# Kernel tuning notes

Hardware: AMD Instinct MI355X
Metric: run time of the kernel (lower is better)

## Reference

```python
import jax, jax.numpy as jnp
import numpy as np

ROI_SIZE = 14  # hard-coded in the torch module


def _bilinear(feature, x, y):
    """feature: [B,C,H,W]; x, y: arbitrary (matching) shape S of sample coords.
    Returns [B, C, *S]. Matches torch code: corner indices are clamped BEFORE
    the interpolation weights are computed from them."""
    H, W = feature.shape[-2:]
    y1 = jnp.clip(jnp.floor(y).astype(jnp.int32), 0, H - 1)
    y2 = jnp.clip(jnp.floor(y).astype(jnp.int32) + 1, 0, H - 1)
    x1 = jnp.clip(jnp.floor(x).astype(jnp.int32), 0, W - 1)
    x2 = jnp.clip(jnp.floor(x).astype(jnp.int32) + 1, 0, W - 1)
    wx_lo = x - x1  # weight toward x2 column
    wx_hi = x2 - x  # weight toward x1 column
    wy_lo = y - y1
    wy_hi = y2 - y
    p = feature[:, :, y1, x1] * wx_hi + feature[:, :, y1, x2] * wx_lo
    q = feature[:, :, y2, x1] * wx_hi + feature[:, :, y2, x2] * wx_lo
    return p * wy_hi + q * wy_lo


def setup_inputs() -> dict:
    key = jax.random.key(0)
    kf, k1, k2, k3, k4 = jax.random.split(key, 5)
    B, C, H, W, R = 1, 256, 200, 320, 128
    feature = jax.random.normal(kf, (B, C, H, W), dtype=jnp.float32)
    y1 = jax.random.uniform(k1, (R,), minval=0.0, maxval=H * 0.5)
    x1 = jax.random.uniform(k2, (R,), minval=0.0, maxval=W * 0.5)
    hh = jax.random.uniform(k3, (R,), minval=8.0, maxval=H * 0.45)
    ww = jax.random.uniform(k4, (R,), minval=8.0, maxval=W * 0.45)
    rois = jnp.stack([y1, x1, y1 + hh, x1 + ww], axis=-1).astype(jnp.float32)
    return {"feature": feature, "rois": rois}


def reference(feature, rois):
    R = rois.shape[0]
    B, C, H, W = feature.shape
    sh = (rois[:, 2] - rois[:, 0]) / ROI_SIZE  # [R] bin height stride
    sw = (rois[:, 3] - rois[:, 1]) / ROI_SIZE  # [R] bin width stride
    m = jnp.arange(ROI_SIZE, dtype=rois.dtype)
    y_base = rois[:, 0:1] + sh[:, None] * m  # [R, M]
    x_base = rois[:, 1:2] + sw[:, None] * m  # [R, N]
    frac = jnp.array([1.0 / 3.0, 2.0 / 3.0], dtype=rois.dtype)
    ys = y_base[:, :, None] + sh[:, None, None] * frac  # [R, M, 2]
    xs = x_base[:, :, None] + sw[:, None, None] * frac  # [R, N, 2]
    # all 4 (y, x) sample-point combos per bin -> [R, M, N, 2, 2]
    yy = jnp.broadcast_to(ys[:, :, None, :, None], (R, ROI_SIZE, ROI_SIZE, 2, 2))
    xx = jnp.broadcast_to(xs[:, None, :, None, :], (R, ROI_SIZE, ROI_SIZE, 2, 2))
    samples = _bilinear(feature, xx, yy)  # [B, C, R, M, N, 2, 2]
    # Faithful to torch.max(tensor) with NO dim: global max over B, C, R and
    # the 4 sample points, giving one scalar per bin (m, n).
    bin_max = jnp.max(samples, axis=(0, 1, 2, 5, 6))  # [M, N]
    return jnp.broadcast_to(bin_max, (R, C, ROI_SIZE, ROI_SIZE))
```

## Files before the change

kernel.cpp:

```cpp
#include <hip/hip_runtime.h>
#include <float.h>
#include <stdint.h>

#define CC 256
#define HH 200
#define WW 320
#define HW (HH * WW)
#define MM 14
#define NCH 8
#define CG 4
#define CPB (CC / CG)
#define SP4 38
#define SPF (SP4 * 4)

__global__ void roi_init(float* __restrict__ binmax) {
    int t = blockIdx.x * blockDim.x + threadIdx.x;
    if (t < MM * MM) binmax[t] = -FLT_MAX;
}

__device__ inline void atomicMaxF(float* addr, float val) {
    if (val >= 0.0f) {
        atomicMax((int*)addr, __float_as_int(val));
    } else {
        atomicMin((unsigned int*)addr, __float_as_uint(val));
    }
}

__device__ __forceinline__ void gload_lds16(const float* g, float* l) {
    __builtin_amdgcn_global_load_lds(
        (const __attribute__((address_space(1))) unsigned int*)g,
        (__attribute__((address_space(3))) unsigned int*)l,
        16, 0, 0);
}

__global__ __launch_bounds__(256, 8) void roi_reduce(
    const float* __restrict__ feature,
    const float* __restrict__ rois,
    float* __restrict__ binmax)
{
    const int bid = blockIdx.x;
    const int cg  = bid & (CG - 1);
    const int rm  = bid >> 2;
    const int m   = rm % MM;
    const int r   = rm / MM;
    const int tid = threadIdx.x;
    const int cbase = cg * CPB;

    const float ry1 = rois[r * 4 + 0];
    const float rx1 = rois[r * 4 + 1];
    const float ry2 = rois[r * 4 + 2];
    const float rx2 = rois[r * 4 + 3];
    const float sh = (ry2 - ry1) * (1.0f / 14.0f);
    const float sw = (rx2 - rx1) * (1.0f / 14.0f);
    const float f13 = 1.0f / 3.0f, f23 = 2.0f / 3.0f;

    const float yA = ry1 + sh * (float)m + sh * f13;
    const float yB = ry1 + sh * (float)m + sh * f23;
    const int y1A = min(max((int)floorf(yA), 0), HH - 1);
    const int y2A = min(max((int)floorf(yA) + 1, 0), HH - 1);
    const int y1B = min(max((int)floorf(yB), 0), HH - 1);
    const int y2B = min(max((int)floorf(yB) + 1, 0), HH - 1);
    const float wyloA = yA - (float)y1A, wyhiA = (float)y2A - yA;
    const float wyloB = yB - (float)y1B, wyhiB = (float)y2B - yB;

    const float xmin = rx1 + sw * f13;
    const float xmax = rx1 + sw * 13.0f + sw * f23;
    int xlo = min(max((int)floorf(xmin), 0), WW - 1);
    int xhi = min(max((int)floorf(xmax) + 1, 0), WW - 1);
    const int xlo4 = xlo & ~3;
    int span = xhi - xlo4 + 1;
    if (span > 4 * SP4 - 4) span = 4 * SP4 - 4;
    const int span4 = (span + 3) >> 2;

    const int s  = tid % 56;
    const int cs = tid / 56;
    const int n  = s >> 2;
    const int j  = (s >> 1) & 1;
    const int i  = s & 1;
    const bool active = (tid < 224);

    float wxlo = 0.f, wxhi = 0.f, wylo = 0.f, wyhi = 0.f;
    int c0 = 0, c1 = 0, ra = 0, rb = 1;
    if (active) {
        float x = rx1 + sw * (float)n + sw * (j ? f23 : f13);
        int x1c = min(max((int)floorf(x), 0), WW - 1);
        int x2c = min(max((int)floorf(x) + 1, 0), WW - 1);
        wxlo = x - (float)x1c;
        wxhi = (float)x2c - x;
        c0 = min(max(x1c - xlo4, 0), span - 1);
        c1 = min(max(x2c - xlo4, 0), span - 1);
        if (i == 0) { ra = 0; rb = 1; wylo = wyloA; wyhi = wyhiA; }
        else        { ra = 2; rb = 3; wylo = wyloB; wyhi = wyhiB; }
    }

    __shared__ float tileF[NCH][4][SPF];
    __shared__ float pmax[224];

    const int rg   = tid >> 6;
    const int lane = tid & 63;
    const int myrow = (rg == 0) ? y1A : (rg == 1) ? y2A : (rg == 2) ? y1B : y2B;
    const float* gRow = feature + cbase * HW + myrow * WW + xlo4 + (lane << 2);
    const bool ld = lane < span4;

    float lmax = -FLT_MAX;

    for (int cc = 0; cc < CPB; cc += NCH) {
        __syncthreads();
        if (ld) {
            const float* g = gRow + (size_t)cc * HW;
            #pragma unroll
            for (int ch = 0; ch < NCH; ++ch) {
                gload_lds16(g, &tileF[ch][rg][0]);
                g += HW;
            }
        }
        __syncthreads();
        if (active) {
            #pragma unroll
            for (int q = 0; q < 2; ++q) {
                const int ch = cs * 2 + q;
                float v11 = tileF[ch][ra][c0];
                float v12 = tileF[ch][ra][c1];
                float v21 = tileF[ch][rb][c0];
                float v22 = tileF[ch][rb][c1];
                float p  = v11 * wxhi + v12 * wxlo;
                float q2 = v21 * wxhi + v22 * wxlo;
                lmax = fmaxf(lmax, p * wyhi + q2 * wylo);
            }
        }
    }

    if (active) pmax[tid] = lmax;
    __syncthreads();
    if (tid < MM) {
        float v = -FLT_MAX;
        #pragma unroll
        for (int c4 = 0; c4 < 4; ++c4)
            #pragma unroll
            for (int q4 = 0; q4 < 4; ++q4)
                v = fmaxf(v, pmax[c4 * 56 + tid * 4 + q4]);
        atomicMaxF(&binmax[m * MM + tid], v);
    }
}

__global__ __launch_bounds__(256) void roi_bcast(
    const float* __restrict__ binmax, float4* __restrict__ out, int total4)
{
    __shared__ float4 b4[49];
    int t = threadIdx.x;
    if (t < 49) b4[t] = ((const float4*)binmax)[t];
    __syncthreads();
    const int stride = gridDim.x * 256;
    for (int idx = blockIdx.x * 256 + t; idx < total4; idx += stride)
        out[idx] = b4[idx % 49];
}

extern "C" void kernel_launch(void* const* d_in, const int* in_sizes, int n_in,
                              void* d_out, int out_size, void* d_ws, size_t ws_size,
                              hipStream_t stream) {
    const float* feature = (const float*)d_in[0];
    const float* rois    = (const float*)d_in[1];
    float* binmax = (float*)d_ws;
    float* out    = (float*)d_out;

    const int R = in_sizes[1] / 4;

    roi_init<<<1, 256, 0, stream>>>(binmax);
    roi_reduce<<<R * MM * CG, 256, 0, stream>>>(feature, rois, binmax);

    const int total4 = out_size / 4;
    int nb = (total4 + 255) / 256;
    if (nb > 2048) nb = 2048;
    roi_bcast<<<nb, 256, 0, stream>>>(binmax, (float4*)out, total4);
}
```

Baseline: 162.2 us.

## Register-prefetch feature tiles with flat thread-to-slice load mapping

Replaces the direct global-to-LDS loads, which were issued per row group by lanes below span4, with a flattened mapping. All 256 threads cooperatively load (channel, row, column4) slices into registers. The next chunk's global loads are issued right after storing the current chunk to LDS, overlapping memory latency with compute, and the barriers become raw s_barrier calls with explicit waitcnts. It also packs LDS addressing into precomputed offsets and handles the clamped-equal-column case with a select. This costs extra VGPRs for five float4 buffers, which may lower occupancy under the 8-wave launch bound.

```diff
diff --git a/kernel.cpp b/kernel.cpp
--- a/kernel.cpp
+++ b/kernel.cpp
@@ -1,6 +1,5 @@
 #include <hip/hip_runtime.h>
 #include <float.h>
-#include <stdint.h>
 
 #define CC 256
 #define HH 200
@@ -10,8 +9,10 @@
 #define NCH 8
 #define CG 4
 #define CPB (CC / CG)
-#define SP4 38
-#define SPF (SP4 * 4)
+#define NR (CPB / NCH)
+#define SPF 152
+#define NSLICE (NCH * 4)
+#define MAXSLOT 5
 
 __global__ void roi_init(float* __restrict__ binmax) {
     int t = blockIdx.x * blockDim.x + threadIdx.x;
@@ -24,13 +25,6 @@
     } else {
         atomicMin((unsigned int*)addr, __float_as_uint(val));
     }
-}
-
-__device__ __forceinline__ void gload_lds16(const float* g, float* l) {
-    __builtin_amdgcn_global_load_lds(
-        (const __attribute__((address_space(1))) unsigned int*)g,
-        (__attribute__((address_space(3))) unsigned int*)l,
-        16, 0, 0);
 }
 
 __global__ __launch_bounds__(256, 8) void roi_reduce(
@@ -69,7 +63,7 @@
     int xhi = min(max((int)floorf(xmax) + 1, 0), WW - 1);
     const int xlo4 = xlo & ~3;
     int span = xhi - xlo4 + 1;
-    if (span > 4 * SP4 - 4) span = 4 * SP4 - 4;
+    if (span > 4 * 37 - 3) span = 4 * 37 - 3;
     const int span4 = (span + 3) >> 2;
 
     const int s  = tid % 56;
@@ -80,55 +74,102 @@
     const bool active = (tid < 224);
 
     float wxlo = 0.f, wxhi = 0.f, wylo = 0.f, wyhi = 0.f;
-    int c0 = 0, c1 = 0, ra = 0, rb = 1;
+    int aoff0 = 0, aoff1 = 0;
+    bool csel = false;
     if (active) {
         float x = rx1 + sw * (float)n + sw * (j ? f23 : f13);
         int x1c = min(max((int)floorf(x), 0), WW - 1);
         int x2c = min(max((int)floorf(x) + 1, 0), WW - 1);
         wxlo = x - (float)x1c;
         wxhi = (float)x2c - x;
-        c0 = min(max(x1c - xlo4, 0), span - 1);
-        c1 = min(max(x2c - xlo4, 0), span - 1);
-        if (i == 0) { ra = 0; rb = 1; wylo = wyloA; wyhi = wyhiA; }
-        else        { ra = 2; rb = 3; wylo = wyloB; wyhi = wyhiB; }
-    }
-
-    __shared__ float tileF[NCH][4][SPF];
+        int c0 = min(max(x1c - xlo4, 0), span - 1);
+        csel = (x2c == x1c);
+        int ra;
+        if (i == 0) { ra = 0; wylo = wyloA; wyhi = wyhiA; }
+        else        { ra = 2; wylo = wyloB; wyhi = wyhiB; }
+        const int ch0 = cs * 2;
+        aoff0 = (ch0 * 4 + ra) * SPF + c0;
+        aoff1 = aoff0 + 4 * SPF;
+    }
+
+    __shared__ float tile[NSLICE * SPF];
     __shared__ float pmax[224];
 
-    const int rg   = tid >> 6;
-    const int lane = tid & 63;
-    const int myrow = (rg == 0) ? y1A : (rg == 1) ? y2A : (rg == 2) ? y1B : y2B;
-    const float* gRow = feature + cbase * HW + myrow * WW + xlo4 + (lane << 2);
-    const bool ld = lane < span4;
-
+    const int o0 = y1A * WW, o1 = y2A * WW, o2 = y1B * WW, o3 = y2B * WW;
+    const int T = NSLICE * span4;
+    const char* fbase = (const char*)(feature + (size_t)cbase * HW);
+
+    unsigned gvoff[MAXSLOT];
+    int      loff[MAXSLOT];
+    bool     val[MAXSLOT];
+    #pragma unroll
+    for (int q = 0; q < MAXSLOT; ++q) {
+        int t = tid + 256 * q;
+        bool v = (t < T);
+        val[q] = v;
+        int tt = v ? t : 0;
+        int slice = tt / span4;
+        int c4    = tt - slice * span4;
+        int ch    = slice >> 2;
+        int row   = slice & 3;
+        int rowoff = o0;
+        rowoff = (row == 1) ? o1 : rowoff;
+        rowoff = (row == 2) ? o2 : rowoff;
+        rowoff = (row == 3) ? o3 : rowoff;
+        gvoff[q] = (unsigned)((ch * HW + rowoff + xlo4 + c4 * 4) * 4);
+        loff[q]  = slice * SPF + c4 * 4;
+    }
+
+    typedef float f4v __attribute__((ext_vector_type(4)));
+    f4v d[MAXSLOT];
+
+    #define ISSUE(kk) do {                                                   \
+        const char* fb_ = fbase + (size_t)(kk) * NCH * HW * 4;               \
+        _Pragma("unroll")                                                    \
+        for (int q = 0; q < MAXSLOT; ++q)                                    \
+            if (val[q]) d[q] = *(const f4v*)(fb_ + gvoff[q]);                \
+    } while (0)
+
+    ISSUE(0);
     float lmax = -FLT_MAX;
 
-    for (int cc = 0; cc < CPB; cc += NCH) {
-        __syncthreads();
-        if (ld) {
-            const float* g = gRow + (size_t)cc * HW;
-            #pragma unroll
-            for (int ch = 0; ch < NCH; ++ch) {
-                gload_lds16(g, &tileF[ch][rg][0]);
-                g += HW;
+    for (int k = 0; k < NR; ++k) {
+        asm volatile("s_waitcnt vmcnt(0)" ::: "memory");
+        __builtin_amdgcn_s_barrier();
+        asm volatile("" ::: "memory");
+
+        #pragma unroll
+        for (int q = 0; q < MAXSLOT; ++q)
+            if (val[q]) *(f4v*)&tile[loff[q]] = d[q];
+
+        if (k + 1 < NR) ISSUE(k + 1);
+
+        asm volatile("s_waitcnt lgkmcnt(0)" ::: "memory");
+        __builtin_amdgcn_s_barrier();
+        asm volatile("" ::: "memory");
+
+        if (active) {
+            {
+                const float* a = &tile[aoff0];
+                float v11 = a[0], v21 = a[SPF];
+                float v12 = a[1], v22 = a[SPF + 1];
+                if (csel) { v12 = v11; v22 = v21; }
+                float p  = v11 * wxhi + v12 * wxlo;
+                float qq = v21 * wxhi + v22 * wxlo;
+                lmax = fmaxf(lmax, p * wyhi + qq * wylo);
+            }
+            {
+                const float* a = &tile[aoff1];
+                float v11 = a[0], v21 = a[SPF];
+                float v12 = a[1], v22 = a[SPF + 1];
+                if (csel) { v12 = v11; v22 = v21; }
+                float p  = v11 * wxhi + v12 * wxlo;
+                float qq = v21 * wxhi + v22 * wxlo;
+                lmax = fmaxf(lmax, p * wyhi + qq * wylo);
             }
         }
-        __syncthreads();
-        if (active) {
-            #pragma unroll
-            for (int q = 0; q < 2; ++q) {
-                const int ch = cs * 2 + q;
-                float v11 = tileF[ch][ra][c0];
-                float v12 = tileF[ch][ra][c1];
-                float v21 = tileF[ch][rb][c0];
-                float v22 = tileF[ch][rb][c1];
-                float p  = v11 * wxhi + v12 * wxlo;
-                float q2 = v21 * wxhi + v22 * wxlo;
-                lmax = fmaxf(lmax, p * wyhi + q2 * wylo);
-            }
-        }
-    }
+    }
+    #undef ISSUE
 
     if (active) pmax[tid] = lmax;
     __syncthreads();
```

Result: faster. 138.2 us (-14.8%).
